# Optimization experiments

Hardware: AMD Instinct MI355X
Metric: run time of the kernel (lower is better)

Reference implementation:

```python
import jax, jax.numpy as jnp
import numpy as np


def _layer_norm(x, w, b, eps=1e-5):
    mu = jnp.mean(x, axis=-1, keepdims=True)
    var = jnp.mean((x - mu) ** 2, axis=-1, keepdims=True)
    return (x - mu) * jax.lax.rsqrt(var + eps) * w + b


def setup_inputs() -> dict:
    key = jax.random.key(0)
    ks = jax.random.split(key, 6)
    B, S, E, H = 4, 4096, 1024, 16
    dk = E // H            # = n_qubits_transformer = 64
    NQF = 64               # n_qubits_ffn
    x = jax.random.normal(ks[0], (B, S, E), jnp.float32)
    attn_q_params = jax.random.normal(ks[1], (dk, 3), jnp.float32)   # torch.randn init
    out_proj_w = jax.random.normal(ks[2], (E, E), jnp.float32) / np.float32(np.sqrt(E))
    out_proj_b = jnp.zeros((E,), jnp.float32)
    ffn_q_params = jax.random.normal(ks[3], (NQF, 3), jnp.float32)
    ffn_lin_w = jax.random.normal(ks[4], (E, NQF), jnp.float32) / np.float32(np.sqrt(NQF))
    ffn_lin_b = jnp.zeros((E,), jnp.float32)
    return {
        'x': x,
        'attn_q_params': attn_q_params,
        'out_proj_w': out_proj_w,
        'out_proj_b': out_proj_b,
        'ffn_q_params': ffn_q_params,
        'ffn_lin_w': ffn_lin_w,
        'ffn_lin_b': ffn_lin_b,
        'norm1_w': jnp.ones((E,), jnp.float32),
        'norm1_b': jnp.zeros((E,), jnp.float32),
        'norm2_w': jnp.ones((E,), jnp.float32),
        'norm2_b': jnp.zeros((E,), jnp.float32),
    }


def reference(x, attn_q_params, out_proj_w, out_proj_b,
              ffn_q_params, ffn_lin_w, ffn_lin_b,
              norm1_w, norm1_b, norm2_w, norm2_b):
    # Closed form: <Z> = cos(x + a) * cos(b); Rz does not affect <Z>.
    B, S, E = x.shape
    dk = attn_q_params.shape[0]
    H = E // dk
    # ---- quantum multi-head attention (shared QHead params across heads) ----
    heads = x.reshape(B, S, H, dk)                                   # bshd
    z = jnp.cos(heads + attn_q_params[:, 0]) * jnp.cos(attn_q_params[:, 1])
    attn_out = z.reshape(B, S, E) @ out_proj_w.T + out_proj_b
    x1 = _layer_norm(x + attn_out, norm1_w, norm1_b)                 # dropout = identity (eval)
    # ---- quantum feed-forward: encoder uses first n_qubits_ffn features ----
    nq = ffn_q_params.shape[0]
    q = jnp.cos(x1[..., :nq] + ffn_q_params[:, 0]) * jnp.cos(ffn_q_params[:, 1])
    ffn_out = q @ ffn_lin_w.T + ffn_lin_b
    return _layer_norm(x1 + ffn_out, norm2_w, norm2_b)
```

## Files before the change

kernel.cpp:

```cpp
#include <hip/hip_runtime.h>
#include <math.h>

typedef __attribute__((ext_vector_type(8))) short short8;
typedef __attribute__((ext_vector_type(4))) float f32x4;
typedef unsigned short u16;

#define DEV static __device__ __forceinline__

DEV u16 f2bf(float f) {
  union { float f; unsigned u; } v; v.f = f;
  unsigned r = v.u + 0x7FFFu + ((v.u >> 16) & 1u);
  return (u16)(r >> 16);
}
DEV float bf2f(u16 u) {
  union { unsigned u; float f; } v; v.u = ((unsigned)u) << 16;
  return v.f;
}

__global__ __launch_bounds__(256) void k_conv(const float* __restrict__ W,
                                              const float* __restrict__ Wf,
                                              u16* __restrict__ Wb,
                                              u16* __restrict__ Wfb) {
  int i = (blockIdx.x * 256 + threadIdx.x) * 4;
  const int NW = 1024 * 1024;
  if (i < NW) {
    float4 v = *(const float4*)(W + i);
    ushort4 o = {f2bf(v.x), f2bf(v.y), f2bf(v.z), f2bf(v.w)};
    *(ushort4*)(Wb + i) = o;
  } else {
    int j = i - NW;
    float4 v = *(const float4*)(Wf + j);
    ushort4 o = {f2bf(v.x), f2bf(v.y), f2bf(v.z), f2bf(v.w)};
    *(ushort4*)(Wfb + j) = o;
  }
}

__global__ __launch_bounds__(256) void k_zenc(const float* __restrict__ x,
                                              const float* __restrict__ qp,
                                              u16* __restrict__ z) {
  __shared__ float a0[64], c1[64];
  int t = threadIdx.x;
  if (t < 64) { a0[t] = qp[t * 3]; c1[t] = cosf(qp[t * 3 + 1]); }
  __syncthreads();
  size_t i = ((size_t)blockIdx.x * 256 + t) * 4;
  float4 xv = *(const float4*)(x + i);
  int d = (int)(i & 63);
  ushort4 o;
  o.x = f2bf(cosf(xv.x + a0[d + 0]) * c1[d + 0]);
  o.y = f2bf(cosf(xv.y + a0[d + 1]) * c1[d + 1]);
  o.z = f2bf(cosf(xv.z + a0[d + 2]) * c1[d + 2]);
  o.w = f2bf(cosf(xv.w + a0[d + 3]) * c1[d + 3]);
  *(ushort4*)(z + i) = o;
}

__global__ __launch_bounds__(256) void k_gemm(const u16* __restrict__ Z,
                                              const u16* __restrict__ Wb,
                                              const float* __restrict__ x,
                                              const float* __restrict__ opb,
                                              u16* __restrict__ Ybf) {
  constexpr int K = 1024, N = 1024;
  __shared__ __attribute__((aligned(16))) u16 As[2][128 * 32];
  __shared__ __attribute__((aligned(16))) u16 Bs[2][128 * 32];
  int bid = blockIdx.x;
  int wg = (bid & 7) * 128 + (bid >> 3);
  int mt = wg >> 3, nt = wg & 7;
  int m0 = mt * 128, n0 = nt * 128;
  int t = threadIdx.x, lane = t & 63, wv = t >> 6;
  int wr = wv >> 1, wc = wv & 1;

  int kb_log = (t & 3) ^ ((t >> 3) & 3);
  const u16* gA = Z + (size_t)(m0 + (t >> 2)) * K + kb_log * 8;
  const u16* gB = Wb + (size_t)(n0 + (t >> 2)) * K + kb_log * 8;
  int lbase = wv * 512;

  f32x4 acc[4][4];
#pragma unroll
  for (int i = 0; i < 4; ++i)
#pragma unroll
    for (int j = 0; j < 4; ++j) acc[i][j] = (f32x4){0.f, 0.f, 0.f, 0.f};

  auto stage = [&](int buf, int kt) {
    const u16* ga = gA + kt * 32;
    const u16* gb = gB + kt * 32;
#pragma unroll
    for (int j = 0; j < 2; ++j) {
      __builtin_amdgcn_global_load_lds(
          (const __attribute__((address_space(1))) unsigned int*)(ga + (size_t)j * 64 * K),
          (__attribute__((address_space(3))) unsigned int*)&As[buf][j * 2048 + lbase],
          16, 0, 0);
      __builtin_amdgcn_global_load_lds(
          (const __attribute__((address_space(1))) unsigned int*)(gb + (size_t)j * 64 * K),
          (__attribute__((address_space(3))) unsigned int*)&Bs[buf][j * 2048 + lbase],
          16, 0, 0);
    }
  };

  stage(0, 0);
  int cl = lane & 15;
  int kofs = ((lane >> 4) ^ ((lane >> 1) & 3)) * 8;
  int arow = wr * 64 + cl;
  int brow = wc * 64 + cl;
  int cur = 0;
  for (int kt = 0; kt < K / 32; ++kt) {
    __syncthreads();
    if (kt + 1 < K / 32) stage(cur ^ 1, kt + 1);
    short8 av[4], bv[4];
#pragma unroll
    for (int mi = 0; mi < 4; ++mi)
      av[mi] = *(const short8*)&As[cur][(arow + mi * 16) * 32 + kofs];
#pragma unroll
    for (int ni = 0; ni < 4; ++ni)
      bv[ni] = *(const short8*)&Bs[cur][(brow + ni * 16) * 32 + kofs];
#pragma unroll
    for (int mi = 0; mi < 4; ++mi)
#pragma unroll
      for (int ni = 0; ni < 4; ++ni)
        acc[mi][ni] = __builtin_amdgcn_mfma_f32_16x16x32_bf16(av[mi], bv[ni], acc[mi][ni], 0, 0, 0);
    cur ^= 1;
  }

  int r0 = m0 + wr * 64 + (lane >> 4) * 4;
  int c0 = n0 + wc * 64 + cl;
#pragma unroll
  for (int mi = 0; mi < 4; ++mi) {
#pragma unroll
    for (int ni = 0; ni < 4; ++ni) {
      int col = c0 + ni * 16;
      float bcol = opb[col];
#pragma unroll
      for (int r = 0; r < 4; ++r) {
        size_t idx = (size_t)(r0 + mi * 16 + r) * N + col;
        Ybf[idx] = f2bf(acc[mi][ni][r] + x[idx] + bcol);
      }
    }
  }
}

__global__ __launch_bounds__(256) void k_ln1(const u16* __restrict__ Ybf,
                                             const float* __restrict__ w1,
                                             const float* __restrict__ b1,
                                             const float* __restrict__ fqp,
                                             u16* __restrict__ X1,
                                             u16* __restrict__ Q) {
  int t = threadIdx.x, lane = t & 63, wv = t >> 6;
  int row = blockIdx.x * 4 + wv;
  size_t base = (size_t)row * 1024 + lane * 16;
  short8 y0 = *(const short8*)&Ybf[base];
  short8 y1 = *(const short8*)&Ybf[base + 8];
  float yv[16];
#pragma unroll
  for (int j = 0; j < 8; ++j) yv[j] = bf2f((u16)y0[j]);
#pragma unroll
  for (int j = 0; j < 8; ++j) yv[8 + j] = bf2f((u16)y1[j]);
  float s = 0.f, s2 = 0.f;
#pragma unroll
  for (int j = 0; j < 16; ++j) { s += yv[j]; s2 += yv[j] * yv[j]; }
#pragma unroll
  for (int msk = 1; msk < 64; msk <<= 1) {
    s += __shfl_xor(s, msk, 64);
    s2 += __shfl_xor(s2, msk, 64);
  }
  float mu = s * (1.f / 1024.f);
  float var = s2 * (1.f / 1024.f) - mu * mu;
  float rs = rsqrtf(var + 1e-5f);

  int col0 = lane * 16;
#pragma unroll
  for (int j = 0; j < 16; ++j)
    yv[j] = (yv[j] - mu) * rs * w1[col0 + j] + b1[col0 + j];
  short8 o0, o1;
#pragma unroll
  for (int j = 0; j < 8; ++j) { o0[j] = (short)f2bf(yv[j]); o1[j] = (short)f2bf(yv[8 + j]); }
  *(short8*)&X1[base] = o0;
  *(short8*)&X1[base + 8] = o1;

  if (lane < 4) {
    short8 q0, q1;
#pragma unroll
    for (int j = 0; j < 16; ++j) {
      int c = col0 + j;
      float qv = cosf(yv[j] + fqp[c * 3]) * cosf(fqp[c * 3 + 1]);
      if (j < 8) q0[j] = (short)f2bf(qv); else q1[j - 8] = (short)f2bf(qv);
    }
    *(short8*)&Q[(size_t)row * 64 + col0] = q0;
    *(short8*)&Q[(size_t)row * 64 + col0 + 8] = q1;
  }
}

__global__ __launch_bounds__(256) void k_ffn(const u16* __restrict__ X1,
                                             const u16* __restrict__ Q,
                                             const u16* __restrict__ Wfb,
                                             const float* __restrict__ fb,
                                             const float* __restrict__ w2,
                                             const float* __restrict__ b2,
                                             float* __restrict__ out) {
  __shared__ float t2[16][1024];
  int t = threadIdx.x, lane = t & 63, wv = t >> 6;
  int m0 = blockIdx.x * 16;
  int kof = (lane >> 4) * 8;
  const short8 a0v = *(const short8*)&Q[(size_t)(m0 + (lane & 15)) * 64 + kof];
  const short8 a1v = *(const short8*)&Q[(size_t)(m0 + (lane & 15)) * 64 + 32 + kof];
  int nbase = wv * 256;
#pragma unroll
  for (int ni = 0; ni < 16; ++ni) {
    int n = nbase + ni * 16 + (lane & 15);
    short8 b0 = *(const short8*)&Wfb[(size_t)n * 64 + kof];
    short8 b1 = *(const short8*)&Wfb[(size_t)n * 64 + 32 + kof];
    f32x4 acc = (f32x4){0.f, 0.f, 0.f, 0.f};
    acc = __builtin_amdgcn_mfma_f32_16x16x32_bf16(a0v, b0, acc, 0, 0, 0);
    acc = __builtin_amdgcn_mfma_f32_16x16x32_bf16(a1v, b1, acc, 0, 0, 0);
#pragma unroll
    for (int r = 0; r < 4; ++r) t2[(lane >> 4) * 4 + r][n] = acc[r];
  }
  __syncthreads();
  for (int rr = 0; rr < 4; ++rr) {
    int row = wv * 4 + rr;
    size_t grow = (size_t)(m0 + row) * 1024;
    float vv[16];
    float s = 0.f, s2 = 0.f;
#pragma unroll
    for (int j = 0; j < 16; ++j) {
      int col = j * 64 + lane;
      float val = bf2f(X1[grow + col]) + t2[row][col] + fb[col];
      vv[j] = val; s += val; s2 += val * val;
    }
#pragma unroll
    for (int m = 1; m < 64; m <<= 1) { s += __shfl_xor(s, m, 64); s2 += __shfl_xor(s2, m, 64); }
    float mu = s * (1.f / 1024.f);
    float var = s2 * (1.f / 1024.f) - mu * mu;
    float rs = rsqrtf(var + 1e-5f);
#pragma unroll
    for (int j = 0; j < 16; ++j) {
      int col = j * 64 + lane;
      out[grow + col] = (vv[j] - mu) * rs * w2[col] + b2[col];
    }
  }
}

extern "C" void kernel_launch(void* const* d_in, const int* in_sizes, int n_in,
                              void* d_out, int out_size, void* d_ws, size_t ws_size,
                              hipStream_t stream) {
  const float* x   = (const float*)d_in[0];
  const float* aqp = (const float*)d_in[1];
  const float* opw = (const float*)d_in[2];
  const float* opb = (const float*)d_in[3];
  const float* fqp = (const float*)d_in[4];
  const float* flw = (const float*)d_in[5];
  const float* flb = (const float*)d_in[6];
  const float* n1w = (const float*)d_in[7];
  const float* n1b = (const float*)d_in[8];
  const float* n2w = (const float*)d_in[9];
  const float* n2b = (const float*)d_in[10];
  float* out = (float*)d_out;

  char* ws = (char*)d_ws;
  u16* zbuf = (u16*)(ws + 0);
  u16* Wb   = (u16*)(ws + 33554432);
  u16* Wfb  = (u16*)(ws + 35651584);
  u16* Qb   = (u16*)(ws + 35782656);

  u16* Ybf = (u16*)d_out;

  k_conv<<<1088, 256, 0, stream>>>(opw, flw, Wb, Wfb);
  k_zenc<<<16384, 256, 0, stream>>>(x, aqp, zbuf);
  k_gemm<<<1024, 256, 0, stream>>>(zbuf, Wb, x, opb, Ybf);
  k_ln1<<<4096, 256, 0, stream>>>(Ybf, n1w, n1b, fqp, zbuf , Qb);
  k_ffn<<<1024, 256, 0, stream>>>(zbuf, Qb, Wfb, flb, n2w, n2b, out);
}
```

Before: 155.6 us.

## Rewrite attention GEMM as 256x256 tile, 8-wave, 4-stage pipelined kernel

Replaces the 128x128 double-buffered bf16 GEMM with a 256x256 tile computed by 8 waves. It uses a 4-unit LDS ring of 32-wide K slices, explicit vmcnt/lgkmcnt waits, barriers and s_setprio around the MFMA bursts. Loads are staged ahead and interleaved with MFMA half-steps. The goal is to raise arithmetic intensity, cut global traffic and hide load latency. It costs much more LDS (128 KB) and registers, so occupancy is limited, and only 256 blocks are launched on a GPU with many CUs.

```diff
diff --git a/kernel.cpp b/kernel.cpp
--- a/kernel.cpp
+++ b/kernel.cpp
@@ -5,7 +5,14 @@
 typedef __attribute__((ext_vector_type(4))) float f32x4;
 typedef unsigned short u16;
 
+#define AS1 __attribute__((address_space(1)))
+#define AS3 __attribute__((address_space(3)))
 #define DEV static __device__ __forceinline__
+#define MFMA_(a, b, c) __builtin_amdgcn_mfma_f32_16x16x32_bf16(a, b, c, 0, 0, 0)
+#define BAR() __builtin_amdgcn_s_barrier()
+#define LGKM0() asm volatile("s_waitcnt lgkmcnt(0)" ::: "memory")
+#define VMC(n) asm volatile("s_waitcnt vmcnt(" #n ")" ::: "memory")
+#define SETP(p) __builtin_amdgcn_s_setprio(p)
 
 DEV u16 f2bf(float f) {
   union { float f; unsigned u; } v; v.f = f;
@@ -53,83 +60,146 @@
   *(ushort4*)(z + i) = o;
 }
 
-__global__ __launch_bounds__(256) void k_gemm(const u16* __restrict__ Z,
-                                              const u16* __restrict__ Wb,
-                                              const float* __restrict__ x,
-                                              const float* __restrict__ opb,
-                                              u16* __restrict__ Ybf) {
-  constexpr int K = 1024, N = 1024;
-  __shared__ __attribute__((aligned(16))) u16 As[2][128 * 32];
-  __shared__ __attribute__((aligned(16))) u16 Bs[2][128 * 32];
-  int bid = blockIdx.x;
-  int wg = (bid & 7) * 128 + (bid >> 3);
-  int mt = wg >> 3, nt = wg & 7;
-  int m0 = mt * 128, n0 = nt * 128;
-  int t = threadIdx.x, lane = t & 63, wv = t >> 6;
-  int wr = wv >> 1, wc = wv & 1;
-
-  int kb_log = (t & 3) ^ ((t >> 3) & 3);
-  const u16* gA = Z + (size_t)(m0 + (t >> 2)) * K + kb_log * 8;
-  const u16* gB = Wb + (size_t)(n0 + (t >> 2)) * K + kb_log * 8;
-  int lbase = wv * 512;
-
-  f32x4 acc[4][4];
-#pragma unroll
-  for (int i = 0; i < 4; ++i)
+template <int P>
+DEV void mm2(f32x4 (&acc)[8][4], const short8 (&av)[8], short8 b0, short8 b1) {
+#pragma unroll
+  for (int mi = 0; mi < 8; ++mi) {
+    acc[mi][2 * P]     = MFMA_(av[mi], b0, acc[mi][2 * P]);
+    acc[mi][2 * P + 1] = MFMA_(av[mi], b1, acc[mi][2 * P + 1]);
+  }
+}
+
+__global__ __launch_bounds__(512, 2) void k_gemm(const u16* __restrict__ Z,
+                                                 const u16* __restrict__ Wb,
+                                                 const float* __restrict__ x,
+                                                 const float* __restrict__ opb,
+                                                 u16* __restrict__ Ybf) {
+  __shared__ __attribute__((aligned(16))) u16 Alds[2][2][8192];
+  __shared__ __attribute__((aligned(16))) u16 Blds[2][2][8192];
+  const int bid = blockIdx.x;
+  const int mt = (bid & 7) * 8 + ((bid >> 3) & 7);
+  const int nt = bid >> 6;
+  const int m0 = mt * 256, n0 = nt * 256;
+  const int t = threadIdx.x, lane = t & 63, wv = t >> 6;
+  const int wm = wv >> 2, wn = wv & 3;
+  const int cl = lane & 15, kq = lane >> 4;
+
+  const int gsw = kq ^ (cl & 3) ^ ((cl >> 2) & 3);
+  const int aoff = (wm * 128 + cl) * 32 + gsw * 8;
+  const int boff = (wn * 64 + cl) * 32 + gsw * 8;
+
+  const int r0 = t >> 2;
+  const int kgs = (t & 3) ^ (r0 & 3) ^ ((r0 >> 2) & 3);
+  const size_t st0 = (size_t)r0 * 1024 + kgs * 8;
+  const size_t st1 = st0 + (size_t)128 * 1024;
+  const int d0 = wv * 512, d1 = 4096 + wv * 512;
+
+  u16* const A00 = &Alds[0][0][0]; u16* const A01 = &Alds[0][1][0];
+  u16* const A10 = &Alds[1][0][0]; u16* const A11 = &Alds[1][1][0];
+  u16* const B00 = &Blds[0][0][0]; u16* const B01 = &Blds[0][1][0];
+  u16* const B10 = &Blds[1][0][0]; u16* const B11 = &Blds[1][1][0];
+
+  const u16* const zb = Z + (size_t)m0 * 1024;
+  const u16* const wbp = Wb + (size_t)n0 * 1024;
+
+  auto stage = [&](u16* unit, const u16* g0) {
+    __builtin_amdgcn_global_load_lds((const AS1 unsigned int*)(g0 + st0),
+                                     (AS3 unsigned int*)(unit + d0), 16, 0, 0);
+    __builtin_amdgcn_global_load_lds((const AS1 unsigned int*)(g0 + st1),
+                                     (AS3 unsigned int*)(unit + d1), 16, 0, 0);
+  };
+
+  f32x4 acc[8][4];
+#pragma unroll
+  for (int i = 0; i < 8; ++i)
 #pragma unroll
     for (int j = 0; j < 4; ++j) acc[i][j] = (f32x4){0.f, 0.f, 0.f, 0.f};
-
-  auto stage = [&](int buf, int kt) {
-    const u16* ga = gA + kt * 32;
-    const u16* gb = gB + kt * 32;
-#pragma unroll
-    for (int j = 0; j < 2; ++j) {
-      __builtin_amdgcn_global_load_lds(
-          (const __attribute__((address_space(1))) unsigned int*)(ga + (size_t)j * 64 * K),
-          (__attribute__((address_space(3))) unsigned int*)&As[buf][j * 2048 + lbase],
-          16, 0, 0);
-      __builtin_amdgcn_global_load_lds(
-          (const __attribute__((address_space(1))) unsigned int*)(gb + (size_t)j * 64 * K),
-          (__attribute__((address_space(3))) unsigned int*)&Bs[buf][j * 2048 + lbase],
-          16, 0, 0);
-    }
+  short8 av[8];
+
+  auto rdA = [&](const u16* unit) {
+#pragma unroll
+    for (int mi = 0; mi < 8; ++mi)
+      av[mi] = *(const short8*)&unit[aoff + mi * 512];
   };
 
-  stage(0, 0);
-  int cl = lane & 15;
-  int kofs = ((lane >> 4) ^ ((lane >> 1) & 3)) * 8;
-  int arow = wr * 64 + cl;
-  int brow = wc * 64 + cl;
-  int cur = 0;
-  for (int kt = 0; kt < K / 32; ++kt) {
-    __syncthreads();
-    if (kt + 1 < K / 32) stage(cur ^ 1, kt + 1);
-    short8 av[4], bv[4];
-#pragma unroll
-    for (int mi = 0; mi < 4; ++mi)
-      av[mi] = *(const short8*)&As[cur][(arow + mi * 16) * 32 + kofs];
-#pragma unroll
-    for (int ni = 0; ni < 4; ++ni)
-      bv[ni] = *(const short8*)&Bs[cur][(brow + ni * 16) * 32 + kofs];
-#pragma unroll
-    for (int mi = 0; mi < 4; ++mi)
-#pragma unroll
-      for (int ni = 0; ni < 4; ++ni)
-        acc[mi][ni] = __builtin_amdgcn_mfma_f32_16x16x32_bf16(av[mi], bv[ni], acc[mi][ni], 0, 0, 0);
-    cur ^= 1;
-  }
-
-  int r0 = m0 + wr * 64 + (lane >> 4) * 4;
-  int c0 = n0 + wc * 64 + cl;
-#pragma unroll
-  for (int mi = 0; mi < 4; ++mi) {
+  stage(A00, zb);      stage(B00, wbp);
+  stage(A01, zb + 32); stage(B01, wbp + 32);
+  stage(A10, zb + 64); stage(B10, wbp + 64);
+  stage(A11, zb + 96);
+  VMC(10);
+  BAR();
+
+  short8 b0, b1;
+#pragma unroll 1
+  for (int I = 0; I < 7; ++I) {
+    const u16* zt = zb + I * 128;
+    const u16* wt = wbp + I * 128;
+    rdA(A00);
+    b0 = *(const short8*)&B00[boff]; b1 = *(const short8*)&B00[boff + 512];
+    stage(B11, wt + 96);
+    BAR(); SETP(1); mm2<0>(acc, av, b0, b1); SETP(0); LGKM0(); BAR();
+    b0 = *(const short8*)&B00[boff + 1024]; b1 = *(const short8*)&B00[boff + 1536];
+    stage(A00, zt + 128);
+    BAR(); SETP(1); mm2<1>(acc, av, b0, b1); SETP(0); LGKM0(); VMC(10); BAR();
+    rdA(A01);
+    b0 = *(const short8*)&B01[boff]; b1 = *(const short8*)&B01[boff + 512];
+    stage(B00, wt + 128);
+    BAR(); SETP(1); mm2<0>(acc, av, b0, b1); SETP(0); LGKM0(); BAR();
+    b0 = *(const short8*)&B01[boff + 1024]; b1 = *(const short8*)&B01[boff + 1536];
+    stage(A01, zt + 160);
+    BAR(); SETP(1); mm2<1>(acc, av, b0, b1); SETP(0); LGKM0(); VMC(10); BAR();
+    rdA(A10);
+    b0 = *(const short8*)&B10[boff]; b1 = *(const short8*)&B10[boff + 512];
+    stage(B01, wt + 160);
+    BAR(); SETP(1); mm2<0>(acc, av, b0, b1); SETP(0); LGKM0(); BAR();
+    b0 = *(const short8*)&B10[boff + 1024]; b1 = *(const short8*)&B10[boff + 1536];
+    stage(A10, zt + 192);
+    BAR(); SETP(1); mm2<1>(acc, av, b0, b1); SETP(0); LGKM0(); VMC(10); BAR();
+    rdA(A11);
+    b0 = *(const short8*)&B11[boff]; b1 = *(const short8*)&B11[boff + 512];
+    stage(B10, wt + 192);
+    BAR(); SETP(1); mm2<0>(acc, av, b0, b1); SETP(0); LGKM0(); BAR();
+    b0 = *(const short8*)&B11[boff + 1024]; b1 = *(const short8*)&B11[boff + 1536];
+    stage(A11, zt + 224);
+    BAR(); SETP(1); mm2<1>(acc, av, b0, b1); SETP(0); LGKM0(); VMC(10); BAR();
+  }
+
+  {
+    const u16* wt = wbp + 7 * 128;
+    rdA(A00);
+    b0 = *(const short8*)&B00[boff]; b1 = *(const short8*)&B00[boff + 512];
+    stage(B11, wt + 96);
+    BAR(); SETP(1); mm2<0>(acc, av, b0, b1); SETP(0); LGKM0(); BAR();
+    b0 = *(const short8*)&B00[boff + 1024]; b1 = *(const short8*)&B00[boff + 1536];
+    BAR(); SETP(1); mm2<1>(acc, av, b0, b1); SETP(0); LGKM0(); VMC(8); BAR();
+    rdA(A01);
+    b0 = *(const short8*)&B01[boff]; b1 = *(const short8*)&B01[boff + 512];
+    BAR(); SETP(1); mm2<0>(acc, av, b0, b1); SETP(0); LGKM0(); BAR();
+    b0 = *(const short8*)&B01[boff + 1024]; b1 = *(const short8*)&B01[boff + 1536];
+    BAR(); SETP(1); mm2<1>(acc, av, b0, b1); SETP(0); LGKM0(); VMC(4); BAR();
+    rdA(A10);
+    b0 = *(const short8*)&B10[boff]; b1 = *(const short8*)&B10[boff + 512];
+    BAR(); SETP(1); mm2<0>(acc, av, b0, b1); SETP(0); LGKM0(); BAR();
+    b0 = *(const short8*)&B10[boff + 1024]; b1 = *(const short8*)&B10[boff + 1536];
+    BAR(); SETP(1); mm2<1>(acc, av, b0, b1); SETP(0); LGKM0(); VMC(0); BAR();
+    rdA(A11);
+    b0 = *(const short8*)&B11[boff]; b1 = *(const short8*)&B11[boff + 512];
+    BAR(); SETP(1); mm2<0>(acc, av, b0, b1); SETP(0); LGKM0(); BAR();
+    b0 = *(const short8*)&B11[boff + 1024]; b1 = *(const short8*)&B11[boff + 1536];
+    BAR(); SETP(1); mm2<1>(acc, av, b0, b1); SETP(0); LGKM0(); BAR();
+  }
+
+  const int rb = m0 + wm * 128 + kq * 4;
+  const int cb = n0 + wn * 64 + cl;
+#pragma unroll
+  for (int mi = 0; mi < 8; ++mi) {
 #pragma unroll
     for (int ni = 0; ni < 4; ++ni) {
-      int col = c0 + ni * 16;
+      int col = cb + ni * 16;
       float bcol = opb[col];
 #pragma unroll
       for (int r = 0; r < 4; ++r) {
-        size_t idx = (size_t)(r0 + mi * 16 + r) * N + col;
+        size_t idx = (size_t)(rb + mi * 16 + r) * 1024 + col;
         Ybf[idx] = f2bf(acc[mi][ni][r] + x[idx] + bcol);
       }
     }
@@ -204,11 +274,11 @@
 #pragma unroll
   for (int ni = 0; ni < 16; ++ni) {
     int n = nbase + ni * 16 + (lane & 15);
-    short8 b0 = *(const short8*)&Wfb[(size_t)n * 64 + kof];
-    short8 b1 = *(const short8*)&Wfb[(size_t)n * 64 + 32 + kof];
+    short8 bb0 = *(const short8*)&Wfb[(size_t)n * 64 + kof];
+    short8 bb1 = *(const short8*)&Wfb[(size_t)n * 64 + 32 + kof];
     f32x4 acc = (f32x4){0.f, 0.f, 0.f, 0.f};
-    acc = __builtin_amdgcn_mfma_f32_16x16x32_bf16(a0v, b0, acc, 0, 0, 0);
-    acc = __builtin_amdgcn_mfma_f32_16x16x32_bf16(a1v, b1, acc, 0, 0, 0);
+    acc = MFMA_(a0v, bb0, acc);
+    acc = MFMA_(a1v, bb1, acc);
 #pragma unroll
     for (int r = 0; r < 4; ++r) t2[(lane >> 4) * 4 + r][n] = acc[r];
   }
@@ -263,7 +333,7 @@
 
   k_conv<<<1088, 256, 0, stream>>>(opw, flw, Wb, Wfb);
   k_zenc<<<16384, 256, 0, stream>>>(x, aqp, zbuf);
-  k_gemm<<<1024, 256, 0, stream>>>(zbuf, Wb, x, opb, Ybf);
+  k_gemm<<<256, 512, 0, stream>>>(zbuf, Wb, x, opb, Ybf);
   k_ln1<<<4096, 256, 0, stream>>>(Ybf, n1w, n1b, fqp, zbuf , Qb);
   k_ffn<<<1024, 256, 0, stream>>>(zbuf, Qb, Wfb, flb, n2w, n2b, out);
 }
```

Result: faster. 141.8 us (-8.9%).
